# Optimization experiments

Hardware: AMD Instinct MI355X
Metric: run time of the kernel (lower is better)

## Reference

```python
import jax, jax.numpy as jnp
import numpy as np

DIM_M = 512
NEG_INF = -1e30


def setup_inputs() -> dict:
    key = jax.random.key(0)
    k1, k2, k3, k4, k5, k6, k7 = jax.random.split(key, 7)
    B, Lc, Lq, d = 16, 1024, 512, DIM_M
    C = jax.random.normal(k1, (B, Lc, d), dtype=jnp.float32)
    Q = jax.random.normal(k2, (B, Lq, d), dtype=jnp.float32)
    cmask = jax.random.randint(k3, (B, Lc), 0, 2).astype(jnp.float32)
    qmask = jax.random.randint(k4, (B, Lq), 0, 2).astype(jnp.float32)
    lim = np.sqrt(1.0 / d)
    w = jax.random.uniform(k5, (3 * d,), minval=-lim, maxval=lim, dtype=jnp.float32)
    # out_linear: Linear(4d -> d), torch default init
    bound = np.sqrt(1.0 / (4 * d))
    out_w = jax.random.uniform(k6, (d, 4 * d), minval=-bound, maxval=bound, dtype=jnp.float32)
    out_b = jax.random.uniform(k7, (d,), minval=-bound, maxval=bound, dtype=jnp.float32)
    return {"C": C, "Q": Q, "cmask": cmask, "qmask": qmask, "w": w, "out_w": out_w, "out_b": out_b}


def _mask_logits(t, m):
    return t * m + (1.0 - m) * NEG_INF


def reference(C, Q, cmask, qmask, w, out_w, out_b):
    d = C.shape[-1]
    w1, w2, w3 = w[:d], w[d:2 * d], w[2 * d:]
    # Decomposed trilinear similarity (same math as cat([Ct,Qt,Ct*Qt]) @ w):
    # S[b,i,j] = C[b,i]@w1 + Q[b,j]@w2 + (C[b,i]*w3) @ Q[b,j]
    S = (C @ w1)[:, :, None] + (Q @ w2)[:, None, :] \
        + jnp.einsum('bid,bjd->bij', C * w3, Q)  # [B, Lc, Lq]
    qm = qmask[:, None, :]  # [B, 1, Lq]
    cm = cmask[:, :, None]  # [B, Lc, 1]
    S1 = jax.nn.softmax(_mask_logits(S, qm), axis=2)  # over Lq
    S2 = jax.nn.softmax(_mask_logits(S, cm), axis=1)  # over Lc
    A = jnp.einsum('bij,bjd->bid', S1, Q)  # [B, Lc, d]
    # bmm(bmm(S1, S2^T), C) == S1 @ (S2^T @ C) by associativity (cheaper)
    S2TC = jnp.einsum('bij,bid->bjd', S2, C)  # [B, Lq, d]
    Bm = jnp.einsum('bij,bjd->bid', S1, S2TC)  # [B, Lc, d]
    out = jnp.concatenate([C, A, C * A, C * Bm], axis=2)  # [B, Lc, 4d]
    # dropout inactive (inference); out_linear
    return out @ out_w.T + out_b
```

## Files before the change

### kernel.cpp

```cpp
#include <hip/hip_runtime.h>
#include <hip/hip_bf16.h>


#define NB 16
#define LC 1024
#define LQ 512
#define DM 512
#define D4 2048
#define NEGINF (-1e30f)
#define LDA32 40

typedef __bf16 v8bf __attribute__((ext_vector_type(8)));
typedef __bf16 v4bf __attribute__((ext_vector_type(4)));
typedef float  v4f  __attribute__((ext_vector_type(4)));

#define MFMA16 __builtin_amdgcn_mfma_f32_16x16x32_bf16

#define GLOAD16(gp, lp) __builtin_amdgcn_global_load_lds( \
    (const __attribute__((address_space(1))) void*)(gp), \
    (__attribute__((address_space(3))) void*)(lp), 16, 0, 0)

#define TILE_SETUP8 \
  const int t = threadIdx.x, lane = t & 63, wave = t >> 6; \
  const int wm = wave >> 2, wn = wave & 3, quad = lane >> 4, col = lane & 15; \
  const int sr = t >> 2;

#define ZERO_ACC8 \
  v4f acc[4][2]; \
  _Pragma("unroll") for (int x = 0; x < 4; ++x) \
  _Pragma("unroll") for (int y = 0; y < 2; ++y) \
  _Pragma("unroll") for (int r = 0; r < 4; ++r) acc[x][y][r] = 0.f;

#define FRAG_MMA8S(AL, BL, LDA, KO) do { \
  v8bf af_[4], bf_[2]; \
  _Pragma("unroll") for (int x = 0; x < 4; ++x) \
    af_[x] = *(const v8bf*)&AL[(wm * 64 + x * 16 + col) * LDA + KO + quad * 8]; \
  _Pragma("unroll") for (int y = 0; y < 2; ++y) \
    bf_[y] = *(const v8bf*)&BL[(wn * 32 + y * 16 + col) * LDA + KO + quad * 8]; \
  _Pragma("unroll") for (int x = 0; x < 4; ++x) \
  _Pragma("unroll") for (int y = 0; y < 2; ++y) \
    acc[x][y] = MFMA16(af_[x], bf_[y], acc[x][y], 0, 0, 0); \
} while (0)

#define GEMM_PROLOG \
  __shared__ __bf16 Al[128 * 64], Bl[128 * 64]; \
  int bx = blockIdx.x, by = blockIdx.y, bz = blockIdx.z; \
  xcd_remap(bx, by, bz); \
  const int b = bz, i0 = by * 128, n0 = bx * 128; \
  const int t = threadIdx.x, lane = t & 63, wave = t >> 6; \
  const int wm = wave >> 1, wn = wave & 1, quad = lane >> 4, col = lane & 15; \
  const int srow = wave * 32 + (lane >> 3), scol = (lane & 7) * 8; \
  v4f acc[4][4]; \
  _Pragma("unroll") for (int x = 0; x < 4; ++x) \
  _Pragma("unroll") for (int y = 0; y < 4; ++y) \
  _Pragma("unroll") for (int r = 0; r < 4; ++r) acc[x][y][r] = 0.f;

#define GEMM_KLOOP(Arow, Brow, LDGA, LDGB, KEXT) \
  for (int k0 = 0; k0 < (KEXT); k0 += 64) { \
    _Pragma("unroll") for (int u = 0; u < 4; ++u) { \
      GLOAD16(Arow + (size_t)(u * 8) * (LDGA) + k0, &Al[(wave * 32 + u * 8) * 64]); \
      GLOAD16(Brow + (size_t)(u * 8) * (LDGB) + k0, &Bl[(wave * 32 + u * 8) * 64]); \
    } \
    __syncthreads(); \
    _Pragma("unroll") for (int ko = 0; ko < 2; ++ko) { \
      v8bf af_[4], bf_[4]; \
      _Pragma("unroll") for (int x = 0; x < 4; ++x) \
        af_[x] = *(const v8bf*)&Al[(wm * 64 + x * 16 + col) * 64 + ko * 32 + quad * 8]; \
      _Pragma("unroll") for (int y = 0; y < 4; ++y) \
        bf_[y] = *(const v8bf*)&Bl[(wn * 64 + y * 16 + col) * 64 + ko * 32 + quad * 8]; \
      _Pragma("unroll") for (int x = 0; x < 4; ++x) \
      _Pragma("unroll") for (int y = 0; y < 4; ++y) \
        acc[x][y] = MFMA16(af_[x], bf_[y], acc[x][y], 0, 0, 0); \
    } \
    __syncthreads(); \
  }

__device__ __forceinline__ void xcd_remap(int& bx, int& by, int& bz) {
  const int gx = gridDim.x, gy = gridDim.y, gz = gridDim.z;
  int flat = bx + gx * (by + gy * bz);
  int per = (gx * gy * gz) >> 3;
  int nw = (flat & 7) * per + (flat >> 3);
  bx = nw % gx;
  int r = nw / gx;
  by = r % gy;
  bz = r / gy;
}

__device__ __forceinline__ v8bf cvt8f(float4 a, float4 b) {
  v8bf h;
  h[0] = (__bf16)a.x; h[1] = (__bf16)a.y; h[2] = (__bf16)a.z; h[3] = (__bf16)a.w;
  h[4] = (__bf16)b.x; h[5] = (__bf16)b.y; h[6] = (__bf16)b.z; h[7] = (__bf16)b.w;
  return h;
}

__global__ void k_rowdots(const float* __restrict__ C, const float* __restrict__ Q,
                          const float* __restrict__ w,
                          float* __restrict__ cw1, float* __restrict__ qw2,
                          __bf16* __restrict__ Cbf, __bf16* __restrict__ Qw3) {
  const int wid = threadIdx.x >> 6, lane = threadIdx.x & 63;
  const int row = blockIdx.x * 4 + wid;
  const bool isC = row < NB * LC;
  const int lr = isC ? row : row - NB * LC;
  const float* src = (isC ? C : Q) + (size_t)lr * DM;
  const float* wv  = isC ? w : (w + DM);
  const float* w3  = w + 2 * DM;
  __bf16* dst = (isC ? Cbf : Qw3) + (size_t)lr * DM;
  float v = 0.f;
#pragma unroll
  for (int s = 0; s < 2; ++s) {
    const int k = lane * 4 + s * 256;
    float4 f = *(const float4*)(src + k);
    float4 g = *(const float4*)(wv + k);
    v += f.x * g.x + f.y * g.y + f.z * g.z + f.w * g.w;
    v4bf h;
    if (isC) {
      h[0] = (__bf16)f.x; h[1] = (__bf16)f.y; h[2] = (__bf16)f.z; h[3] = (__bf16)f.w;
    } else {
      float4 s3 = *(const float4*)(w3 + k);
      h[0] = (__bf16)(f.x * s3.x); h[1] = (__bf16)(f.y * s3.y);
      h[2] = (__bf16)(f.z * s3.z); h[3] = (__bf16)(f.w * s3.w);
    }
    *(v4bf*)(dst + k) = h;
  }
#pragma unroll
  for (int off = 32; off; off >>= 1) v += __shfl_down(v, off, 64);
  if (lane == 0) {
    if (isC) cw1[row] = v;
    else     qw2[lr] = v;
  }
}

__global__ void k_transpose(const float* __restrict__ in, __bf16* __restrict__ outT,
                            int R, int Cd) {
  __shared__ __bf16 tile[64][66];
  const int b = blockIdx.z;
  const int r0 = blockIdx.y * 64, c0 = blockIdx.x * 64;
  const int tr = threadIdx.x >> 6, tc = threadIdx.x & 63;
  const float* inb = in + (size_t)b * R * Cd;
  __bf16* outb = outT + (size_t)b * Cd * R;
  for (int r = tr; r < 64; r += 4)
    tile[r][tc] = (__bf16)inb[(size_t)(r0 + r) * Cd + c0 + tc];
  __syncthreads();
  for (int c = tr; c < 64; c += 4)
    outb[(size_t)(c0 + c) * R + r0 + tc] = tile[tc][c];
}

__global__ void k_owcvt(const float* __restrict__ OW, __bf16* __restrict__ OWb) {
  size_t i = ((size_t)blockIdx.x * 256 + threadIdx.x) * 4;
  float4 f = *(const float4*)(OW + i);
  v4bf h; h[0] = (__bf16)f.x; h[1] = (__bf16)f.y; h[2] = (__bf16)f.z; h[3] = (__bf16)f.w;
  *(v4bf*)(OWb + i) = h;
}

__global__ __launch_bounds__(256) void k_mfma_S(
    const __bf16* __restrict__ Cbf, const __bf16* __restrict__ Qw3,
    const float* __restrict__ cw1, const float* __restrict__ qw2,
    float* __restrict__ S) {
  GEMM_PROLOG
  const __bf16* Arow = Cbf + (size_t)b * LC * DM + (size_t)(i0 + srow) * DM + scol;
  const __bf16* Brow = Qw3 + (size_t)b * LQ * DM + (size_t)(n0 + srow) * DM + scol;
  GEMM_KLOOP(Arow, Brow, DM, DM, DM)
  float* Sb = S + (size_t)b * LC * LQ;
#pragma unroll
  for (int x = 0; x < 4; ++x) {
    const int mB = i0 + wm * 64 + x * 16 + quad * 4;
    float cv[4];
#pragma unroll
    for (int r = 0; r < 4; ++r) cv[r] = cw1[b * LC + mB + r];
#pragma unroll
    for (int y = 0; y < 4; ++y) {
      const int j = n0 + wn * 64 + y * 16 + col;
      const float qv = qw2[b * LQ + j];
#pragma unroll
      for (int r = 0; r < 4; ++r)
        Sb[(size_t)(mB + r) * LQ + j] = acc[x][y][r] + cv[r] + qv;
    }
  }
}

__global__ __launch_bounds__(1024) void k_softstat(
    const float* __restrict__ S, const float* __restrict__ qmask,
    const float* __restrict__ cmask, __bf16* __restrict__ S1,
    float2* __restrict__ pstat) {
  __shared__ float2 cst[16][LQ];
  const int b = blockIdx.y, ic = blockIdx.x;
  const int tid = threadIdx.x, wv = tid >> 6, lane = tid & 63;
  const float* qm  = qmask + b * LQ;
  const float* cm  = cmask + b * LC + ic * 64;
  const float* Sb  = S  + ((size_t)b * LC + ic * 64) * LQ;
  __bf16*      S1b = S1 + ((size_t)b * LC + ic * 64) * LQ;
  float colm[8], cols[8];
#pragma unroll
  for (int tt = 0; tt < 8; ++tt) { colm[tt] = -3e38f; cols[tt] = 0.f; }
  for (int it = 0; it < 4; ++it) {
    const int r = wv * 4 + it;
    const float cmv = cm[r];
    const float* Srow = Sb + (size_t)r * LQ;
    float sv[8], l1[8];
    float m = -3e38f;
#pragma unroll
    for (int tt = 0; tt < 8; ++tt) {
      int j = lane + 64 * tt;
      sv[tt] = Srow[j];
      float qv = qm[j];
      l1[tt] = qv * sv[tt] + (1.f - qv) * NEGINF;
      m = fmaxf(m, l1[tt]);
    }
#pragma unroll
    for (int off = 32; off; off >>= 1) m = fmaxf(m, __shfl_xor(m, off, 64));
    float e[8], s = 0.f;
#pragma unroll
    for (int tt = 0; tt < 8; ++tt) { e[tt] = __expf(l1[tt] - m); s += e[tt]; }
#pragma unroll
    for (int off = 32; off; off >>= 1) s += __shfl_xor(s, off, 64);
    const float inv = 1.f / s;
#pragma unroll
    for (int tt = 0; tt < 8; ++tt)
      S1b[(size_t)r * LQ + lane + 64 * tt] = (__bf16)(e[tt] * inv);
#pragma unroll
    for (int tt = 0; tt < 8; ++tt) {
      float l2 = cmv * sv[tt] + (1.f - cmv) * NEGINF;
      if (l2 > colm[tt]) { cols[tt] *= __expf(colm[tt] - l2); colm[tt] = l2; }
      cols[tt] += __expf(l2 - colm[tt]);
    }
  }
#pragma unroll
  for (int tt = 0; tt < 8; ++tt) cst[wv][lane + 64 * tt] = make_float2(colm[tt], cols[tt]);
  __syncthreads();
  if (tid < LQ) {
    float M = -3e38f, Sd = 0.f;
#pragma unroll
    for (int k = 0; k < 16; ++k) {
      float2 p = cst[k][tid];
      float nM = fmaxf(M, p.x);
      Sd = Sd * __expf(M - nM) + p.y * __expf(p.x - nM);
      M = nM;
    }
    pstat[((size_t)(b * 16 + ic) * LQ) + tid] = make_float2(M, Sd);
  }
}

__global__ void k_colwrite(const float* __restrict__ S, const float* __restrict__ cmask,
                           const float2* __restrict__ pstat, __bf16* __restrict__ S2T) {
  __shared__ float Mf[64], If[64];
  __shared__ __bf16 tile[64][66];
  const int b = blockIdx.z, ic = blockIdx.y, j0 = blockIdx.x * 64;
  const int c = threadIdx.x & 63, ip = threadIdx.x >> 6;
  if (threadIdx.x < 64) {
    float M = -3e38f, Sd = 0.f;
#pragma unroll
    for (int k = 0; k < 16; ++k) {
      float2 p = pstat[((size_t)(b * 16 + k) * LQ) + j0 + threadIdx.x];
      float nM = fmaxf(M, p.x);
      Sd = Sd * __expf(M - nM) + p.y * __expf(p.x - nM);
      M = nM;
    }
    Mf[threadIdx.x] = M; If[threadIdx.x] = 1.f / Sd;
  }
  __syncthreads();
  const float M = Mf[c], inv = If[c];
  const float* Sb = S + ((size_t)b * LC + ic * 64) * LQ;
  const float* cm = cmask + b * LC + ic * 64;
  for (int r = ip; r < 64; r += 4) {
    float mk = cm[r];
    float logit = mk * Sb[(size_t)r * LQ + j0 + c] + (1.f - mk) * NEGINF;
    tile[r][c] = (__bf16)(__expf(logit - M) * inv);
  }
  __syncthreads();
  __bf16* S2Tb = S2T + ((size_t)b * LQ + j0) * LC + ic * 64;
  for (int jr = ip; jr < 64; jr += 4)
    S2Tb[(size_t)jr * LC + c] = tile[c][jr];
}

__global__ __launch_bounds__(256) void k_mfma_A(
    const __bf16* __restrict__ S1, const __bf16* __restrict__ QT, __bf16* __restrict__ Aw) {
  GEMM_PROLOG
  const __bf16* Arow = S1 + (size_t)b * LC * LQ + (size_t)(i0 + srow) * LQ + scol;
  const __bf16* Brow = QT + (size_t)b * DM * LQ + (size_t)(n0 + srow) * LQ + scol;
  GEMM_KLOOP(Arow, Brow, LQ, LQ, LQ)
  __bf16* Ab = Aw + (size_t)b * LC * DM;
#pragma unroll
  for (int x = 0; x < 4; ++x) {
    const int mB = i0 + wm * 64 + x * 16 + quad * 4;
#pragma unroll
    for (int y = 0; y < 4; ++y) {
      const int n = n0 + wn * 64 + y * 16 + col;
#pragma unroll
      for (int r = 0; r < 4; ++r)
        Ab[(size_t)(mB + r) * DM + n] = (__bf16)acc[x][y][r];
    }
  }
}

__global__ __launch_bounds__(256) void k_mfma_T(
    const __bf16* __restrict__ S2T, const __bf16* __restrict__ CT, __bf16* __restrict__ S2TCT) {
  GEMM_PROLOG
  const int j0 = i0;
  const __bf16* Arow = S2T + (size_t)b * LQ * LC + (size_t)(j0 + srow) * LC + scol;
  const __bf16* Brow = CT  + (size_t)b * DM * LC + (size_t)(n0 + srow) * LC + scol;
  GEMM_KLOOP(Arow, Brow, LC, LC, LC)
#pragma unroll
  for (int x = 0; x < 4; ++x) {
    const int jB = j0 + wm * 64 + x * 16 + quad * 4;
#pragma unroll
    for (int y = 0; y < 4; ++y) {
      const int n = n0 + wn * 64 + y * 16 + col;
      v4bf h;
#pragma unroll
      for (int r = 0; r < 4; ++r) h[r] = (__bf16)acc[x][y][r];
      *(v4bf*)&S2TCT[((size_t)b * DM + n) * LQ + jB] = h;
    }
  }
}

__global__ __launch_bounds__(256) void k_mfma_Bm(
    const __bf16* __restrict__ S1, const __bf16* __restrict__ S2TCT, __bf16* __restrict__ Bmw) {
  GEMM_PROLOG
  const __bf16* Arow = S1    + (size_t)b * LC * LQ + (size_t)(i0 + srow) * LQ + scol;
  const __bf16* Brow = S2TCT + (size_t)b * DM * LQ + (size_t)(n0 + srow) * LQ + scol;
  GEMM_KLOOP(Arow, Brow, LQ, LQ, LQ)
  __bf16* Bb = Bmw + (size_t)b * LC * DM;
#pragma unroll
  for (int x = 0; x < 4; ++x) {
    const int mB = i0 + wm * 64 + x * 16 + quad * 4;
#pragma unroll
    for (int y = 0; y < 4; ++y) {
      const int n = n0 + wn * 64 + y * 16 + col;
#pragma unroll
      for (int r = 0; r < 4; ++r)
        Bb[(size_t)(mB + r) * DM + n] = (__bf16)acc[x][y][r];
    }
  }
}

__global__ __launch_bounds__(512) void k_mfma_out(
    const float* __restrict__ C, const __bf16* __restrict__ Aw, const __bf16* __restrict__ Bmw,
    const __bf16* __restrict__ OWb, const float* __restrict__ ob, float* __restrict__ out) {
  __shared__ __bf16 Asg[4][128 * LDA32], Bsg[4][128 * LDA32];
  int bx = blockIdx.x, by = blockIdx.y, bz = blockIdx.z;
  xcd_remap(bx, by, bz);
  const int b = bz, i0 = by * 128, n0 = bx * 128;
  TILE_SETUP8
  const int skc = (t & 3) * 8;
  const float*  Cr = C   + (size_t)b * LC * DM + (size_t)(i0 + sr) * DM + skc;
  const __bf16* Ar = Aw  + (size_t)b * LC * DM + (size_t)(i0 + sr) * DM + skc;
  const __bf16* Br = Bmw + (size_t)b * LC * DM + (size_t)(i0 + sr) * DM + skc;
  const __bf16* Wr = OWb + (size_t)(n0 + sr) * D4 + skc;
  float4 pc0, pc1; v8bf pA, pB, pw[4];
  auto load = [&](int kl) {
    pc0 = *(const float4*)(Cr + kl); pc1 = *(const float4*)(Cr + kl + 4);
    pA = *(const v8bf*)(Ar + kl);
    pB = *(const v8bf*)(Br + kl);
#pragma unroll
    for (int s = 0; s < 4; ++s) pw[s] = *(const v8bf*)(Wr + s * DM + kl);
  };
  load(0);
  ZERO_ACC8
  for (int kl = 0; kl < DM; kl += 32) {
    float cf[8] = {pc0.x, pc0.y, pc0.z, pc0.w, pc1.x, pc1.y, pc1.z, pc1.w};
    v8bf hC, hCA, hCB;
#pragma unroll
    for (int e = 0; e < 8; ++e) {
      hC[e]  = (__bf16)cf[e];
      hCA[e] = (__bf16)(cf[e] * (float)pA[e]);
      hCB[e] = (__bf16)(cf[e] * (float)pB[e]);
    }
    const int off = sr * LDA32 + skc;
    *(v8bf*)&Asg[0][off] = hC;
    *(v8bf*)&Asg[1][off] = pA;
    *(v8bf*)&Asg[2][off] = hCA;
    *(v8bf*)&Asg[3][off] = hCB;
#pragma unroll
    for (int s = 0; s < 4; ++s) *(v8bf*)&Bsg[s][off] = pw[s];
    __syncthreads();
    int kn = kl + 32; if (kn >= DM) kn = 0;
    load(kn);
#pragma unroll
    for (int s = 0; s < 4; ++s) FRAG_MMA8S(Asg[s], Bsg[s], LDA32, 0);
    __syncthreads();
  }
  float* outb = out + (size_t)b * LC * DM;
#pragma unroll
  for (int x = 0; x < 4; ++x) {
    const int mB = i0 + wm * 64 + x * 16 + quad * 4;
#pragma unroll
    for (int y = 0; y < 2; ++y) {
      const int n = n0 + wn * 32 + y * 16 + col;
      const float bv = ob[n];
#pragma unroll
      for (int r = 0; r < 4; ++r)
        outb[(size_t)(mB + r) * DM + n] = acc[x][y][r] + bv;
    }
  }
}

extern "C" void kernel_launch(void* const* d_in, const int* in_sizes, int n_in,
                              void* d_out, int out_size, void* d_ws, size_t ws_size,
                              hipStream_t stream) {
  const float* C     = (const float*)d_in[0];
  const float* Q     = (const float*)d_in[1];
  const float* cmask = (const float*)d_in[2];
  const float* qmask = (const float*)d_in[3];
  const float* w     = (const float*)d_in[4];
  const float* out_w = (const float*)d_in[5];
  const float* out_b = (const float*)d_in[6];
  float* out = (float*)d_out;

  char* base = (char*)d_ws;
  float*  cw1   = (float*)base;
  float*  qw2   = (float*)(base + 65536);
  char*   R     = base + 131072;
  float*  S     = (float*)R;
  __bf16* Aw    = (__bf16*)R;
  __bf16* CT    = (__bf16*)(R + (16u << 20));
  __bf16* Bmw   = (__bf16*)(R + (16u << 20));
  __bf16* Cbf   = (__bf16*)(base + 131072 + (32u << 20));
  __bf16* S1    = (__bf16*)(base + 131072 + (32u << 20));
  __bf16* Qw3   = (__bf16*)(base + 131072 + (48u << 20));
  __bf16* S2T   = (__bf16*)(base + 131072 + (48u << 20));
  __bf16* OWbf  = S2T;
  char*   Z     = base + 131072 + (64u << 20);
  float2* pstat = (float2*)Z;
  __bf16* QT    = (__bf16*)Z;
  __bf16* S2TCT = (__bf16*)Z;
  (void)in_sizes; (void)n_in; (void)out_size; (void)ws_size;

  k_rowdots<<<(NB * LC + NB * LQ) / 4, 256, 0, stream>>>(C, Q, w, cw1, qw2, Cbf, Qw3);
  k_mfma_S<<<dim3(LQ / 128, LC / 128, NB), 256, 0, stream>>>(Cbf, Qw3, cw1, qw2, S);
  k_softstat<<<dim3(LC / 64, NB), 1024, 0, stream>>>(S, qmask, cmask, S1, pstat);
  k_colwrite<<<dim3(LQ / 64, LC / 64, NB), 256, 0, stream>>>(S, cmask, pstat, S2T);
  k_transpose<<<dim3(DM / 64, LQ / 64, NB), 256, 0, stream>>>(Q, QT, LQ, DM);
  k_transpose<<<dim3(DM / 64, LC / 64, NB), 256, 0, stream>>>(C, CT, LC, DM);
  k_mfma_A<<<dim3(DM / 128, LC / 128, NB), 256, 0, stream>>>(S1, QT, Aw);
  k_mfma_T<<<dim3(DM / 128, LQ / 128, NB), 256, 0, stream>>>(S2T, CT, S2TCT);
  k_owcvt<<<DM * D4 / 1024, 256, 0, stream>>>(out_w, OWbf);
  k_mfma_Bm<<<dim3(DM / 128, LC / 128, NB), 256, 0, stream>>>(S1, S2TCT, Bmw);
  k_mfma_out<<<dim3(DM / 128, LC / 128, NB), 512, 0, stream>>>(C, Aw, Bmw, OWbf, out_b, out);
}
```

Baseline: 277.0 us.

## Move C*A and C*Bm products into GEMM epilogues and unify output GEMM

```diff
diff --git a/kernel.cpp b/kernel.cpp
--- a/kernel.cpp
+++ b/kernel.cpp
@@ -8,7 +8,6 @@
 #define DM 512
 #define D4 2048
 #define NEGINF (-1e30f)
-#define LDA32 40
 
 typedef __bf16 v8bf __attribute__((ext_vector_type(8)));
 typedef __bf16 v4bf __attribute__((ext_vector_type(4)));
@@ -19,28 +18,6 @@
 #define GLOAD16(gp, lp) __builtin_amdgcn_global_load_lds( \
     (const __attribute__((address_space(1))) void*)(gp), \
     (__attribute__((address_space(3))) void*)(lp), 16, 0, 0)
-
-#define TILE_SETUP8 \
-  const int t = threadIdx.x, lane = t & 63, wave = t >> 6; \
-  const int wm = wave >> 2, wn = wave & 3, quad = lane >> 4, col = lane & 15; \
-  const int sr = t >> 2;
-
-#define ZERO_ACC8 \
-  v4f acc[4][2]; \
-  _Pragma("unroll") for (int x = 0; x < 4; ++x) \
-  _Pragma("unroll") for (int y = 0; y < 2; ++y) \
-  _Pragma("unroll") for (int r = 0; r < 4; ++r) acc[x][y][r] = 0.f;
-
-#define FRAG_MMA8S(AL, BL, LDA, KO) do { \
-  v8bf af_[4], bf_[2]; \
-  _Pragma("unroll") for (int x = 0; x < 4; ++x) \
-    af_[x] = *(const v8bf*)&AL[(wm * 64 + x * 16 + col) * LDA + KO + quad * 8]; \
-  _Pragma("unroll") for (int y = 0; y < 2; ++y) \
-    bf_[y] = *(const v8bf*)&BL[(wn * 32 + y * 16 + col) * LDA + KO + quad * 8]; \
-  _Pragma("unroll") for (int x = 0; x < 4; ++x) \
-  _Pragma("unroll") for (int y = 0; y < 2; ++y) \
-    acc[x][y] = MFMA16(af_[x], bf_[y], acc[x][y], 0, 0, 0); \
-} while (0)
 
 #define GEMM_PROLOG \
   __shared__ __bf16 Al[128 * 64], Bl[128 * 64]; \
@@ -86,13 +63,6 @@
   bz = r / gy;
 }
 
-__device__ __forceinline__ v8bf cvt8f(float4 a, float4 b) {
-  v8bf h;
-  h[0] = (__bf16)a.x; h[1] = (__bf16)a.y; h[2] = (__bf16)a.z; h[3] = (__bf16)a.w;
-  h[4] = (__bf16)b.x; h[5] = (__bf16)b.y; h[6] = (__bf16)b.z; h[7] = (__bf16)b.w;
-  return h;
-}
-
 __global__ void k_rowdots(const float* __restrict__ C, const float* __restrict__ Q,
                           const float* __restrict__ w,
                           float* __restrict__ cw1, float* __restrict__ qw2,
@@ -145,11 +115,16 @@
     outb[(size_t)(c0 + c) * R + r0 + tc] = tile[tc][c];
 }
 
-__global__ void k_owcvt(const float* __restrict__ OW, __bf16* __restrict__ OWb) {
+__global__ void k_cvt2(const float* __restrict__ Cf, const float* __restrict__ OW,
+                       __bf16* __restrict__ Cb3, __bf16* __restrict__ OWb) {
+  const size_t NC = (size_t)NB * LC * DM;
   size_t i = ((size_t)blockIdx.x * 256 + threadIdx.x) * 4;
-  float4 f = *(const float4*)(OW + i);
+  const float* src; __bf16* dst; size_t j;
+  if (i < NC) { src = Cf; dst = Cb3; j = i; }
+  else        { src = OW; dst = OWb; j = i - NC; }
+  float4 f = *(const float4*)(src + j);
   v4bf h; h[0] = (__bf16)f.x; h[1] = (__bf16)f.y; h[2] = (__bf16)f.z; h[3] = (__bf16)f.w;
-  *(v4bf*)(OWb + i) = h;
+  *(v4bf*)(dst + j) = h;
 }
 
 __global__ __launch_bounds__(256) void k_mfma_S(
@@ -273,12 +248,15 @@
 }
 
 __global__ __launch_bounds__(256) void k_mfma_A(
-    const __bf16* __restrict__ S1, const __bf16* __restrict__ QT, __bf16* __restrict__ Aw) {
+    const __bf16* __restrict__ S1, const __bf16* __restrict__ QT,
+    const float* __restrict__ Cf, __bf16* __restrict__ Aw, __bf16* __restrict__ CAw) {
   GEMM_PROLOG
   const __bf16* Arow = S1 + (size_t)b * LC * LQ + (size_t)(i0 + srow) * LQ + scol;
   const __bf16* Brow = QT + (size_t)b * DM * LQ + (size_t)(n0 + srow) * LQ + scol;
   GEMM_KLOOP(Arow, Brow, LQ, LQ, LQ)
-  __bf16* Ab = Aw + (size_t)b * LC * DM;
+  const float* Cb = Cf + (size_t)b * LC * DM;
+  __bf16* Ab  = Aw  + (size_t)b * LC * DM;
+  __bf16* CAb = CAw + (size_t)b * LC * DM;
 #pragma unroll
   for (int x = 0; x < 4; ++x) {
     const int mB = i0 + wm * 64 + x * 16 + quad * 4;
@@ -286,8 +264,12 @@
     for (int y = 0; y < 4; ++y) {
       const int n = n0 + wn * 64 + y * 16 + col;
 #pragma unroll
-      for (int r = 0; r < 4; ++r)
-        Ab[(size_t)(mB + r) * DM + n] = (__bf16)acc[x][y][r];
+      for (int r = 0; r < 4; ++r) {
+        const float av = acc[x][y][r];
+        const float cv = Cb[(size_t)(mB + r) * DM + n];
+        Ab[(size_t)(mB + r) * DM + n]  = (__bf16)av;
+        CAb[(size_t)(mB + r) * DM + n] = (__bf16)(av * cv);
+      }
     }
   }
 }
@@ -314,12 +296,14 @@
 }
 
 __global__ __launch_bounds__(256) void k_mfma_Bm(
-    const __bf16* __restrict__ S1, const __bf16* __restrict__ S2TCT, __bf16* __restrict__ Bmw) {
+    const __bf16* __restrict__ S1, const __bf16* __restrict__ S2TCT,
+    const float* __restrict__ Cf, __bf16* __restrict__ CBw) {
   GEMM_PROLOG
   const __bf16* Arow = S1    + (size_t)b * LC * LQ + (size_t)(i0 + srow) * LQ + scol;
   const __bf16* Brow = S2TCT + (size_t)b * DM * LQ + (size_t)(n0 + srow) * LQ + scol;
   GEMM_KLOOP(Arow, Brow, LQ, LQ, LQ)
-  __bf16* Bb = Bmw + (size_t)b * LC * DM;
+  const float* Cb = Cf + (size_t)b * LC * DM;
+  __bf16* CBb = CBw + (size_t)b * LC * DM;
 #pragma unroll
   for (int x = 0; x < 4; ++x) {
     const int mB = i0 + wm * 64 + x * 16 + quad * 4;
@@ -327,65 +311,39 @@
     for (int y = 0; y < 4; ++y) {
       const int n = n0 + wn * 64 + y * 16 + col;
 #pragma unroll
-      for (int r = 0; r < 4; ++r)
-        Bb[(size_t)(mB + r) * DM + n] = (__bf16)acc[x][y][r];
-    }
-  }
-}
-
-__global__ __launch_bounds__(512) void k_mfma_out(
-    const float* __restrict__ C, const __bf16* __restrict__ Aw, const __bf16* __restrict__ Bmw,
-    const __bf16* __restrict__ OWb, const float* __restrict__ ob, float* __restrict__ out) {
-  __shared__ __bf16 Asg[4][128 * LDA32], Bsg[4][128 * LDA32];
-  int bx = blockIdx.x, by = blockIdx.y, bz = blockIdx.z;
-  xcd_remap(bx, by, bz);
-  const int b = bz, i0 = by * 128, n0 = bx * 128;
-  TILE_SETUP8
-  const int skc = (t & 3) * 8;
-  const float*  Cr = C   + (size_t)b * LC * DM + (size_t)(i0 + sr) * DM + skc;
-  const __bf16* Ar = Aw  + (size_t)b * LC * DM + (size_t)(i0 + sr) * DM + skc;
-  const __bf16* Br = Bmw + (size_t)b * LC * DM + (size_t)(i0 + sr) * DM + skc;
-  const __bf16* Wr = OWb + (size_t)(n0 + sr) * D4 + skc;
-  float4 pc0, pc1; v8bf pA, pB, pw[4];
-  auto load = [&](int kl) {
-    pc0 = *(const float4*)(Cr + kl); pc1 = *(const float4*)(Cr + kl + 4);
-    pA = *(const v8bf*)(Ar + kl);
-    pB = *(const v8bf*)(Br + kl);
-#pragma unroll
-    for (int s = 0; s < 4; ++s) pw[s] = *(const v8bf*)(Wr + s * DM + kl);
-  };
-  load(0);
-  ZERO_ACC8
-  for (int kl = 0; kl < DM; kl += 32) {
-    float cf[8] = {pc0.x, pc0.y, pc0.z, pc0.w, pc1.x, pc1.y, pc1.z, pc1.w};
-    v8bf hC, hCA, hCB;
-#pragma unroll
-    for (int e = 0; e < 8; ++e) {
-      hC[e]  = (__bf16)cf[e];
-      hCA[e] = (__bf16)(cf[e] * (float)pA[e]);
-      hCB[e] = (__bf16)(cf[e] * (float)pB[e]);
-    }
-    const int off = sr * LDA32 + skc;
-    *(v8bf*)&Asg[0][off] = hC;
-    *(v8bf*)&Asg[1][off] = pA;
-    *(v8bf*)&Asg[2][off] = hCA;
-    *(v8bf*)&Asg[3][off] = hCB;
-#pragma unroll
-    for (int s = 0; s < 4; ++s) *(v8bf*)&Bsg[s][off] = pw[s];
-    __syncthreads();
-    int kn = kl + 32; if (kn >= DM) kn = 0;
-    load(kn);
-#pragma unroll
-    for (int s = 0; s < 4; ++s) FRAG_MMA8S(Asg[s], Bsg[s], LDA32, 0);
-    __syncthreads();
+      for (int r = 0; r < 4; ++r) {
+        const float cv = Cb[(size_t)(mB + r) * DM + n];
+        CBb[(size_t)(mB + r) * DM + n] = (__bf16)(acc[x][y][r] * cv);
+      }
+    }
+  }
+}
+
+__global__ __launch_bounds__(256) void k_mfma_out(
+    const __bf16* __restrict__ Cb3, const __bf16* __restrict__ Aw,
+    const __bf16* __restrict__ CAw, const __bf16* __restrict__ CBw,
+    const __bf16* __restrict__ OWb, const float* __restrict__ ob,
+    float* __restrict__ out) {
+  GEMM_PROLOG
+  const size_t rowoff = (size_t)b * LC * DM + (size_t)(i0 + srow) * DM + scol;
+  const __bf16* As0 = Cb3 + rowoff;
+  const __bf16* As1 = Aw  + rowoff;
+  const __bf16* As2 = CAw + rowoff;
+  const __bf16* As3 = CBw + rowoff;
+  const __bf16* Brow0 = OWb + (size_t)(n0 + srow) * D4 + scol;
+#pragma unroll
+  for (int seg = 0; seg < 4; ++seg) {
+    const __bf16* Arow = (seg == 0) ? As0 : (seg == 1) ? As1 : (seg == 2) ? As2 : As3;
+    const __bf16* Brow = Brow0 + seg * DM;
+    GEMM_KLOOP(Arow, Brow, DM, D4, DM)
   }
   float* outb = out + (size_t)b * LC * DM;
 #pragma unroll
   for (int x = 0; x < 4; ++x) {
     const int mB = i0 + wm * 64 + x * 16 + quad * 4;
 #pragma unroll
-    for (int y = 0; y < 2; ++y) {
-      const int n = n0 + wn * 32 + y * 16 + col;
+    for (int y = 0; y < 4; ++y) {
+      const int n = n0 + wn * 64 + y * 16 + col;
       const float bv = ob[n];
 #pragma unroll
       for (int r = 0; r < 4; ++r)
@@ -411,29 +369,30 @@
   float*  qw2   = (float*)(base + 65536);
   char*   R     = base + 131072;
   float*  S     = (float*)R;
+  __bf16* CT    = (__bf16*)R;
   __bf16* Aw    = (__bf16*)R;
-  __bf16* CT    = (__bf16*)(R + (16u << 20));
-  __bf16* Bmw   = (__bf16*)(R + (16u << 20));
-  __bf16* Cbf   = (__bf16*)(base + 131072 + (32u << 20));
-  __bf16* S1    = (__bf16*)(base + 131072 + (32u << 20));
-  __bf16* Qw3   = (__bf16*)(base + 131072 + (48u << 20));
-  __bf16* S2T   = (__bf16*)(base + 131072 + (48u << 20));
-  __bf16* OWbf  = S2T;
-  char*   Z     = base + 131072 + (64u << 20);
-  float2* pstat = (float2*)Z;
-  __bf16* QT    = (__bf16*)Z;
-  __bf16* S2TCT = (__bf16*)Z;
+  __bf16* QT    = (__bf16*)(R + (16u << 20));
+  __bf16* CBw   = (__bf16*)(R + (16u << 20));
+  __bf16* Cbf_e = (__bf16*)(R + (32u << 20));
+  __bf16* S1    = (__bf16*)(R + (32u << 20));
+  __bf16* Cbf3  = (__bf16*)(R + (32u << 20));
+  __bf16* Qw3   = (__bf16*)(R + (48u << 20));
+  __bf16* S2T   = (__bf16*)(R + (48u << 20));
+  __bf16* CAw   = (__bf16*)(R + (48u << 20));
+  float2* pstat = (float2*)(R + (64u << 20));
+  __bf16* S2TCT = (__bf16*)(R + (64u << 20));
+  __bf16* OWbf  = (__bf16*)(R + (64u << 20));
   (void)in_sizes; (void)n_in; (void)out_size; (void)ws_size;
 
-  k_rowdots<<<(NB * LC + NB * LQ) / 4, 256, 0, stream>>>(C, Q, w, cw1, qw2, Cbf, Qw3);
-  k_mfma_S<<<dim3(LQ / 128, LC / 128, NB), 256, 0, stream>>>(Cbf, Qw3, cw1, qw2, S);
+  k_rowdots<<<(NB * LC + NB * LQ) / 4, 256, 0, stream>>>(C, Q, w, cw1, qw2, Cbf_e, Qw3);
+  k_mfma_S<<<dim3(LQ / 128, LC / 128, NB), 256, 0, stream>>>(Cbf_e, Qw3, cw1, qw2, S);
   k_softstat<<<dim3(LC / 64, NB), 1024, 0, stream>>>(S, qmask, cmask, S1, pstat);
   k_colwrite<<<dim3(LQ / 64, LC / 64, NB), 256, 0, stream>>>(S, cmask, pstat, S2T);
+  k_transpose<<<dim3(DM / 64, LC / 64, NB), 256, 0, stream>>>(C, CT, LC, DM);
+  k_mfma_T<<<dim3(DM / 128, LQ / 128, NB), 256, 0, stream>>>(S2T, CT, S2TCT);
   k_transpose<<<dim3(DM / 64, LQ / 64, NB), 256, 0, stream>>>(Q, QT, LQ, DM);
-  k_transpose<<<dim3(DM / 64, LC / 64, NB), 256, 0, stream>>>(C, CT, LC, DM);
-  k_mfma_A<<<dim3(DM / 128, LC / 128, NB), 256, 0, stream>>>(S1, QT, Aw);
-  k_mfma_T<<<dim3(DM / 128, LQ / 128, NB), 256, 0, stream>>>(S2T, CT, S2TCT);
-  k_owcvt<<<DM * D4 / 1024, 256, 0, stream>>>(out_w, OWbf);
-  k_mfma_Bm<<<dim3(DM / 128, LC / 128, NB), 256, 0, stream>>>(S1, S2TCT, Bmw);
-  k_mfma_out<<<dim3(DM / 128, LC / 128, NB), 512, 0, stream>>>(C, Aw, Bmw, OWbf, out_b, out);
-}
+  k_mfma_A<<<dim3(DM / 128, LC / 128, NB), 256, 0, stream>>>(S1, QT, C, Aw, CAw);
+  k_mfma_Bm<<<dim3(DM / 128, LC / 128, NB), 256, 0, stream>>>(S1, S2TCT, C, CBw);
+  k_cvt2<<<(NB * LC * DM + DM * D4) / 1024, 256, 0, stream>>>(C, out_w, Cbf3, OWbf);
+  k_mfma_out<<<dim3(DM / 128, LC / 128, NB), 256, 0, stream>>>(Cbf3, Aw, CAw, CBw, OWbf, out_b, out);
+}
```

After: 288.8 us. 1.04x slower.
